# Kernel optimization log

Hardware: AMD Instinct MI355X
Metric: run time of the kernel (lower is better)

Reference implementation:

```python
import jax, jax.numpy as jnp
import numpy as np
from jax import lax

D, R, C = 4, 6, 32
P = 2 * R + 1
N = P * P
MR = 12
MP = 2 * MR + 1
MN = MP * MP


def corr_sampler(f_t, f_r, r, dilate):
    # SpatialCorrelationSampler(kernel_size=1, patch_size=2r+1, dilation_patch=dilate)
    # out[b,py,px,y,x] = sum_c f_t[b,c,y,x] * f_r[b,c, y+(py-r)*dilate, x+(px-r)*dilate] (zero pad)
    b, c, h, w = f_t.shape
    p = 2 * r + 1
    pad = r * dilate
    f_r_p = jnp.pad(f_r, ((0, 0), (0, 0), (pad, pad), (pad, pad)))
    offs = jnp.arange(p, dtype=jnp.int32) * dilate
    ii, jj = jnp.meshgrid(offs, offs, indexing='ij')
    shifts = jnp.stack([ii.ravel(), jj.ravel()], 1)  # (p*p, 2)

    def step(_, ij):
        win = lax.dynamic_slice(f_r_p, (0, 0, ij[0], ij[1]), (b, c, h, w))
        return None, jnp.sum(f_t * win, axis=1)  # (b,h,w)

    _, out = lax.scan(step, None, shifts)  # (p*p, b, h, w)
    return out.transpose(1, 0, 2, 3).reshape(b, p, p, h, w)


def bilinear_sample(im, xs, ys):
    # im: (b,c,H,W); xs, ys: (b,h,w) pixel coords; zero padding outside (grid_sample semantics)
    b, c, H, W = im.shape
    x0 = jnp.floor(xs)
    y0 = jnp.floor(ys)
    out = jnp.zeros((b, c) + xs.shape[1:], im.dtype)
    for dy in (0.0, 1.0):
        for dx in (0.0, 1.0):
            xi = x0 + dx
            yi = y0 + dy
            wgt = (1.0 - jnp.abs(xs - xi)) * (1.0 - jnp.abs(ys - yi))
            valid = (xi >= 0) & (xi <= W - 1) & (yi >= 0) & (yi <= H - 1)
            xc = jnp.clip(xi, 0, W - 1).astype(jnp.int32)
            yc = jnp.clip(yi, 0, H - 1).astype(jnp.int32)
            v = jax.vmap(lambda imb, yb, xb: imb[:, yb, xb])(im, yc, xc)  # (b,c,h,w)
            out = out + v * (wgt * valid.astype(im.dtype))[:, None]
    return out


def deform_im2col(im, offset, r):
    # im: (b,c,h,w); offset: (b,h,w,2) with channels (x, y)
    # returns (b, c, (2r+1)^2, h, w), kernel positions row-major over (ky, kx)
    b, c, H, W = im.shape
    h, w = offset.shape[1], offset.shape[2]
    bx = jnp.arange(W, dtype=im.dtype)[None, None, :] + offset[..., 0]  # (b,h,w)
    by = jnp.arange(H, dtype=im.dtype)[None, :, None] + offset[..., 1]
    ks = jnp.arange(-r, r + 1, dtype=im.dtype)
    ky, kx = jnp.meshgrid(ks, ks, indexing='ij')
    koff = jnp.stack([ky.ravel(), kx.ravel()], 1)  # (N, 2) as (ky, kx)

    def step(_, k):
        return None, bilinear_sample(im, bx + k[1], by + k[0])  # (b,c,h,w)

    _, cols = lax.scan(step, None, koff)  # (N,b,c,h,w)
    return cols.transpose(1, 2, 0, 3, 4)


def unfold(x, r):
    # F.unfold(x, kernel_size=2r+1, padding=r) reshaped to (b,c,N,h,w)
    b, c, h, w = x.shape
    p = 2 * r + 1
    xp = jnp.pad(x, ((0, 0), (0, 0), (r, r), (r, r)))
    iy = jnp.arange(p)[:, None] + jnp.arange(h)[None, :]  # (p,h)
    ix = jnp.arange(p)[:, None] + jnp.arange(w)[None, :]  # (p,w)
    win = xp[:, :, iy[:, None, :, None], ix[None, :, None, :]]  # (b,c,p,p,h,w)
    return win.reshape(b, c, p * p, h, w)


def colorizer_forward(feats_r, feats_t, quantized_r, ref_index, current_ind, dil_int):
    ref_list = [int(v) for v in np.asarray(ref_index)]
    nref = feats_r.shape[0]
    gaps = [int(current_ind) - x for x in ref_list]
    nsearch = len([g for g in gaps if g > int(dil_int)])
    dirates = [min(4, g // int(dil_int) + 1) for g in gaps if g > int(dil_int)]
    b, c, h, w = feats_t.shape

    gy, gx = jnp.meshgrid(jnp.arange(-MR, MR + 1, dtype=feats_t.dtype),
                          jnp.arange(-MR, MR + 1, dtype=feats_t.dtype), indexing='ij')
    grid = jnp.stack([gx, gy], -1).reshape(1, MP, MP, 1, 1, 2)

    corrs = []
    offset0 = None
    for i in range(nsearch):
        cc = corr_sampler(feats_t, feats_r[i], MR, dirates[i])  # (b,MP,MP,h,w)
        cc = jax.nn.softmax(cc.reshape(b, MN, h * w), axis=1)
        cc = cc.reshape(b, MP, MP, h, w, 1)
        # expected displacement (x, y); NOTE: original code keeps only the LAST offset0
        offset0 = (cc * grid).sum(axis=(1, 2)) * dirates[i]  # (b,h,w,2)
        col0 = deform_im2col(feats_r[i], offset0, R)  # (b,c,N,h,w)
        corr = (feats_t[:, :, None] * col0).sum(axis=1).reshape(b, N, h * w)
        corrs.append(corr)
    for i in range(nsearch, nref):
        cr = corr_sampler(feats_t, feats_r[i], R, 1).reshape(b, N, h * w)
        corrs.append(cr)

    corr = jax.nn.softmax(jnp.concatenate(corrs, 1), axis=1)[:, None]  # (b,1,nref*N,hw)

    qr = [quantized_r[i][:, :, ::D, ::D] for i in range(nref)]  # prep: stride D (C!=1)
    cols = [deform_im2col(qr[i], offset0, R).reshape(b, C, N, h * w) for i in range(nsearch)]
    cols += [unfold(qr[i], R).reshape(b, C, N, h * w) for i in range(nsearch, nref)]
    image_uf = jnp.concatenate(cols, 2)  # (b,C,nref*N,hw)

    out = (corr * image_uf).sum(axis=2).reshape(b, C, h, w)
    return out


def setup_inputs() -> dict:
    key = jax.random.key(0)
    k1, k2, k3 = jax.random.split(key, 3)
    feats_r = jax.random.normal(k1, (3, 2, 64, 48, 48), jnp.float32) * 0.1
    feats_t = jax.random.normal(k2, (2, 64, 48, 48), jnp.float32) * 0.1
    quantized_r = jax.random.normal(k3, (3, 2, 32, 192, 192), jnp.float32)
    ref_index = np.array([0, 20, 35], dtype=np.int64)
    return {"feats_r": feats_r, "feats_t": feats_t, "quantized_r": quantized_r,
            "ref_index": ref_index, "current_ind": 40, "dil_int": 15}


def reference(feats_r, feats_t, quantized_r, ref_index, current_ind, dil_int):
    return colorizer_forward(feats_r, feats_t, quantized_r, ref_index, current_ind, dil_int)
```

## Files before the change

kernel.cpp:

```cpp
#include <hip/hip_runtime.h>


typedef unsigned short ushort_t;
typedef unsigned int uint_t;
typedef __attribute__((ext_vector_type(8))) short short8;
typedef __attribute__((ext_vector_type(4))) float f32x4;

namespace {
constexpr int NPIX = 2304;
constexpr int FC   = 64;
constexpr int QC   = 32;

constexpr size_t OFS_FTB  = 0;
constexpr size_t OFS_FRB  = OFS_FTB + (size_t)2*NPIX*FC*2;
constexpr size_t OFS_QRCL = OFS_FRB + (size_t)6*NPIX*FC*2;
constexpr size_t OFS_ACC  = OFS_QRCL + (size_t)6*NPIX*QC*4;
constexpr size_t OFS_CORB = OFS_ACC + (size_t)4*NPIX*16*4;
}

__device__ __forceinline__ ushort_t f2b(float f) {
  uint_t u = __float_as_uint(f);
  return (ushort_t)((u + 0x7fffu + ((u >> 16) & 1u)) >> 16);
}

__global__ __launch_bounds__(256) void pack_all(const float* __restrict__ ft,
                                                const float* __restrict__ fr,
                                                const float* __restrict__ q,
                                                ushort_t* __restrict__ ftb,
                                                ushort_t* __restrict__ frb,
                                                float* __restrict__ qrcl) {
  const int bid = blockIdx.x;
  const int tid = threadIdx.x;
  if (bid < 288) {
    __shared__ float lds[64][65];
    const int mat = bid / 36;
    const int p0  = (bid % 36) * 64;
    const float* src = (mat < 2) ? (ft + (size_t)mat * FC * NPIX)
                                 : (fr + (size_t)(mat - 2) * FC * NPIX);
    ushort_t* dst = (mat < 2) ? (ftb + (size_t)mat * NPIX * FC)
                              : (frb + (size_t)(mat - 2) * NPIX * FC);
    const int lane = tid & 63, row = tid >> 6;
    #pragma unroll
    for (int ch = row; ch < 64; ch += 4)
      lds[ch][lane] = src[(size_t)ch * NPIX + p0 + lane];
    __syncthreads();
    #pragma unroll
    for (int p = row; p < 64; p += 4)
      dst[(size_t)(p0 + p) * FC + lane] = f2b(lds[lane][p]);
  } else {
    __shared__ float lq[32][49];
    const int zz = bid - 288;
    const int ib = zz / 48, yy = zz % 48;
    const float* src = q + (size_t)ib * 32 * 36864 + (size_t)(4 * yy) * 192;
    #pragma unroll
    for (int k = 0; k < 6; ++k) {
      const int l = tid + k * 256;
      const int ch = l / 48, xx = l % 48;
      lq[ch][xx] = src[(size_t)ch * 36864 + 4 * xx];
    }
    __syncthreads();
    float* dst = qrcl + ((size_t)ib * NPIX + yy * 48) * QC;
    #pragma unroll
    for (int k = 0; k < 6; ++k) {
      const int o = tid + k * 256;
      dst[o] = lq[o & 31][o >> 5];
    }
  }
}

template<int MODE>
__device__ __forceinline__ void gram_body(const ushort_t* __restrict__ ftb,
                                          const ushort_t* __restrict__ frb,
                                          float* __restrict__ accb,
                                          float* __restrict__ corb,
                                          int y, int m0, int b, int chunk,
                                          int c0, int c1) {
  constexpr int D_  = (MODE == 0) ? 3 : (MODE == 1) ? 2 : 1;
  constexpr int RAD = (MODE == 2) ? 6 : 12;

  const int lane = threadIdx.x;
  const int col  = lane & 15;
  const int kg   = lane >> 4;

  const short8* ftv = (const short8*)(ftb + ((size_t)b * NPIX + y * 48 + m0 + col) * FC);
  short8 aF0 = ftv[kg];
  short8 aF1 = ftv[4 + kg];

  float wm[3][4], dxv[3][4];
  int sbase[3][4];
  #pragma unroll
  for (int nt = 0; nt < 3; ++nt) {
    #pragma unroll
    for (int r = 0; r < 4; ++r) {
      const int xr   = m0 + kg * 4 + r;
      const int diff = nt * 16 + col - xr;
      const int qd   = diff / D_;
      const bool v   = (diff % D_ == 0) && (qd >= -RAD) && (qd <= RAD);
      wm[nt][r]  = v ? 1.f : 0.f;
      dxv[nt][r] = (float)qd;
      if (MODE == 2) sbase[nt][r] = ((int)b * NPIX + y * 48 + xr) * 169 + (qd + 6);
    }
  }

  const ushort_t* frmat = frb + (size_t)(MODE * 2 + b) * NPIX * FC;
  float se[4] = {0,0,0,0}, sx[4] = {0,0,0,0}, sy[4] = {0,0,0,0};

  for (int dy = c0; dy < c1; ++dy) {
    const int yyr = y + (dy - RAD) * D_;
    if (yyr < 0 || yyr >= 48) continue;
    const float dyv = (float)(dy - RAD);
    const short8* frow = (const short8*)(frmat + (size_t)yyr * 48 * FC);
    #pragma unroll
    for (int nt = 0; nt < 3; ++nt) {
      const short8* bp = frow + (size_t)(nt * 16 + col) * 8;
      short8 b0 = bp[kg], b1 = bp[4 + kg];
      f32x4 c = {0.f, 0.f, 0.f, 0.f};
      c = __builtin_amdgcn_mfma_f32_16x16x32_bf16(aF0, b0, c, 0, 0, 0);
      c = __builtin_amdgcn_mfma_f32_16x16x32_bf16(aF1, b1, c, 0, 0, 0);
      if (MODE < 2) {
        #pragma unroll
        for (int r = 0; r < 4; ++r) {
          const float e = __expf(c[r]) * wm[nt][r];
          se[r] += e;
          sx[r] = fmaf(e, dxv[nt][r], sx[r]);
          sy[r] = fmaf(e, dyv, sy[r]);
        }
      } else {
        #pragma unroll
        for (int r = 0; r < 4; ++r)
          if (wm[nt][r] != 0.f) corb[sbase[nt][r] + dy * 13] = c[r];
      }
    }
  }

  if (MODE < 2) {
    #pragma unroll
    for (int r = 0; r < 4; ++r) {
      #pragma unroll
      for (int m = 1; m <= 8; m <<= 1) {
        se[r] += __shfl_xor(se[r], m);
        sx[r] += __shfl_xor(sx[r], m);
        sy[r] += __shfl_xor(sy[r], m);
      }
    }
    if (col == 0) {
      #pragma unroll
      for (int r = 0; r < 4; ++r) {
        const int p = y * 48 + m0 + kg * 4 + r;
        float* a = accb + ((size_t)(MODE * 2 + b) * NPIX + p) * 16 + chunk * 3;
        a[0] = se[r]; a[1] = sx[r]; a[2] = sy[r];
      }
    }
  }
}

__global__ __launch_bounds__(64) void gram_kernel(const ushort_t* __restrict__ ftb,
                                                  const ushort_t* __restrict__ frb,
                                                  float* __restrict__ accb,
                                                  float* __restrict__ corb) {
  const int y  = ((blockIdx.x & 7) * 6) + (blockIdx.x >> 3);
  const int m0 = blockIdx.y * 16;
  const int z  = blockIdx.z;
  if (z < 10) {
    const int b = z / 5, chunk = z % 5;
    gram_body<0>(ftb, frb, accb, corb, y, m0, b, chunk, chunk * 5, chunk * 5 + 5);
  } else if (z < 20) {
    const int zz = z - 10;
    const int b = zz / 5, chunk = zz % 5;
    gram_body<1>(ftb, frb, accb, corb, y, m0, b, chunk, chunk * 5, chunk * 5 + 5);
  } else {
    const int zz = z - 20;
    const int b = zz / 3, chunk = zz % 3;
    const int c0 = (chunk == 0) ? 0 : (chunk == 1) ? 5 : 9;
    const int c1 = (chunk == 0) ? 5 : (chunk == 1) ? 9 : 13;
    gram_body<2>(ftb, frb, accb, corb, y, m0, b, chunk, c0, c1);
  }
}

__global__ __launch_bounds__(128, 6) void fuse_kernel(const ushort_t* __restrict__ ftb,
                                                      const ushort_t* __restrict__ frb,
                                                      const float* __restrict__ accb,
                                                      const float* __restrict__ corb,
                                                      const float* __restrict__ qrcl,
                                                      float* __restrict__ out) {
  const int tid = threadIdx.x;
  const int wv = tid >> 6, lane = tid & 63;
  const int b = blockIdx.y;
  const int bsw = ((blockIdx.x & 7) * 144) + (blockIdx.x >> 3);
  const int pix = bsw * 2 + wv;
  const int x = pix % 48, y = pix / 48;

  __shared__ __align__(16) float sDu[2][416];
  __shared__ float sp[2][512];
  __shared__ int   gaddr[2][224];
  __shared__ float gw0[2][224], gw1[2][224];

  const int kgB = lane >> 4;
  const short8* ftv = (const short8*)(ftb + ((size_t)b * NPIX + pix) * FC);
  const short8 bF0 = ftv[kgB], bF1 = ftv[4 + kgB];

  float cv5 = 0.f, cv6 = 0.f, cv7 = 0.f;
  {
    const float* cb = corb + ((size_t)b * NPIX + pix) * 169;
    int n = lane - 18;
    if (n >= 0) {
      const int yy = y + n / 13 - 6, xx = x + n % 13 - 6;
      if (yy >= 0 && yy < 48 && xx >= 0 && xx < 48) cv5 = cb[n];
    }
    n = lane + 46;
    {
      const int yy = y + n / 13 - 6, xx = x + n % 13 - 6;
      if (yy >= 0 && yy < 48 && xx >= 0 && xx < 48) cv6 = cb[n];
    }
    n = lane + 110;
    if (n < 169) {
      const int yy = y + n / 13 - 6, xx = x + n % 13 - 6;
      if (yy >= 0 && yy < 48 && xx >= 0 && xx < 48) cv7 = cb[n];
    }
  }

  float vox = 0.f, voy = 0.f;
  if (lane < 2) {
    const int d = (lane == 0) ? 3 : 2;
    const float4* a4 = (const float4*)(accb + ((size_t)(lane * 2 + b) * NPIX + pix) * 16);
    float t[16];
    *(float4*)&t[0]  = a4[0]; *(float4*)&t[4]  = a4[1];
    *(float4*)&t[8]  = a4[2]; *(float4*)&t[12] = a4[3];
    float se = t[0] + t[3] + t[6] + t[9] + t[12];
    float sx = t[1] + t[4] + t[7] + t[10] + t[13];
    float sy = t[2] + t[5] + t[8] + t[11] + t[14];
    const int klox = max(-12, -(x / d)), khix = min(12, (47 - x) / d);
    const int kloy = max(-12, -(y / d)), khiy = min(12, (47 - y) / d);
    const int nvx = khix - klox + 1, nvy = khiy - kloy + 1;
    const int svx = (klox + khix) * nvx / 2, svy = (kloy + khiy) * nvy / 2;
    se += (float)(625 - nvx * nvy);
    sx -= (float)(nvy * svx);
    sy -= (float)(nvx * svy);
    vox = (float)d * sx / se;
    voy = (float)d * sy / se;
  }
  const float ox0 = __shfl(vox, 0), oy0 = __shfl(voy, 0);
  const float ox1 = __shfl(vox, 1), oy1 = __shfl(voy, 1);

  const float bxf0 = floorf((float)x + ox0), byf0 = floorf((float)y + oy0);
  const float bxf1 = floorf((float)x + ox1), byf1 = floorf((float)y + oy1);
  const float fx0 = (float)x + ox0 - bxf0, fy0 = (float)y + oy0 - byf0;
  const float fx1 = (float)x + ox1 - bxf1, fy1 = (float)y + oy1 - byf1;
  const int bx00 = (int)bxf0 - 6, by00 = (int)byf0 - 6;
  const int bx01 = (int)bxf1 - 6, by01 = (int)byf1 - 6;

  {
    const int arow = lane & 15, kg = lane >> 4;
    const short8 z8 = {0,0,0,0,0,0,0,0};
    float* sDw = sDu[wv];
    #pragma unroll 2
    for (int gi = 0; gi < 26; ++gi) {
      const bool r1 = gi >= 13;
      const int grp = r1 ? gi - 13 : gi;
      const int g = grp * 16 + arow;
      short8 a0 = z8, a1 = z8;
      if (g < 196) {
        const int gy = (r1 ? by01 : by00) + g / 14;
        const int gx = (r1 ? bx01 : bx00) + g % 14;
        if (gy >= 0 && gy < 48 && gx >= 0 && gx < 48) {
          const short8* fp = (const short8*)(frb + ((size_t)((r1 ? 2 : 0) + b) * NPIX + gy * 48 + gx) * FC);
          a0 = fp[kg]; a1 = fp[4 + kg];
        }
      }
      f32x4 c = {0.f, 0.f, 0.f, 0.f};
      c = __builtin_amdgcn_mfma_f32_16x16x32_bf16(a0, bF0, c, 0, 0, 0);
      c = __builtin_amdgcn_mfma_f32_16x16x32_bf16(a1, bF1, c, 0, 0, 0);
      if (arow == 0)
        *(f32x4*)&sDw[(r1 ? 208 : 0) + grp * 16 + kg * 4] = c;
    }
  }
  __syncthreads();

  float ls = 0.f;
  {
    float* spw = sp[wv];
    const float* sD0 = sDu[wv];
    const float* sD1 = sDu[wv] + 208;
    #pragma unroll
    for (int k = 0; k < 8; ++k) {
      const int s = lane + 64 * k;
      if (s < 507) {
        float v;
        if (s < 338) {
          const bool r1 = (s >= 169);
          const unsigned n = r1 ? s - 169 : s;
          const float fx = r1 ? fx1 : fx0, fy = r1 ? fy1 : fy0;
          const float w00 = (1.f - fy) * (1.f - fx), w01 = (1.f - fy) * fx;
          const float w10 = fy * (1.f - fx),        w11 = fy * fx;
          const unsigned a_ = n / 13u, c2 = n % 13u;
          const float* Dp = r1 ? sD1 : sD0;
          v = w00 * Dp[a_ * 14 + c2]       + w01 * Dp[a_ * 14 + c2 + 1]
            + w10 * Dp[(a_ + 1) * 14 + c2] + w11 * Dp[(a_ + 1) * 14 + c2 + 1];
        } else {
          v = (k == 5) ? cv5 : (k == 6) ? cv6 : cv7;
        }
        const float e = __expf(v);
        spw[s] = e; ls += e;
      }
    }
  }
  #pragma unroll
  for (int o = 1; o <= 32; o <<= 1) ls += __shfl_xor(ls, o);
  const float inv = 1.f / ls;
  __syncthreads();

  int*   gaddr2 = (int*)sDu[wv];
  float* gwq2   = sDu[wv] + 208;
  {
    const float* spw = sp[wv];
    const float w00 = (1.f - fy1) * (1.f - fx1), w01 = (1.f - fy1) * fx1;
    const float w10 = fy1 * (1.f - fx1),        w11 = fy1 * fx1;
    #pragma unroll
    for (int j = 0; j < 4; ++j) {
      const int t = lane + 64 * j;
      if (t < 224) {
        if (t < 196) {
          const int ty = t / 14, tx = t % 14;
          auto P = [&](const float* base, int a, int c2) -> float {
            return (a >= 0 && a < 13 && c2 >= 0 && c2 < 13) ? base[a * 13 + c2] : 0.f;
          };
          const float s0 = w00 * P(spw, ty, tx)     + w01 * P(spw, ty, tx - 1)
                         + w10 * P(spw, ty - 1, tx) + w11 * P(spw, ty - 1, tx - 1);
          const float s1 = w00 * P(spw + 169, ty, tx)     + w01 * P(spw + 169, ty, tx - 1)
                         + w10 * P(spw + 169, ty - 1, tx) + w11 * P(spw + 169, ty - 1, tx - 1);
          const int gy = by01 + ty, gx = bx01 + tx;
          const bool v = (gy >= 0 && gy < 48 && gx >= 0 && gx < 48);
          gaddr[wv][t] = v ? (gy * 48 + gx) * QC : 0;
          gw0[wv][t] = v ? s0 : 0.f;
          gw1[wv][t] = v ? s1 : 0.f;
        } else {
          gaddr[wv][t] = 0; gw0[wv][t] = 0.f; gw1[wv][t] = 0.f;
        }
      }
    }
    #pragma unroll
    for (int j = 0; j < 3; ++j) {
      const int t = lane + 64 * j;
      if (t < 169) {
        const int yy = y + t / 13 - 6, xx = x + t % 13 - 6;
        const bool v = (yy >= 0 && yy < 48 && xx >= 0 && xx < 48);
        gaddr2[t] = v ? (yy * 48 + xx) * QC : 0;
        gwq2[t] = v ? spw[338 + t] : 0.f;
      } else {
        gaddr2[t] = 0; gwq2[t] = 0.f;
      }
    }
  }
  __syncthreads();

  const int chgrp = lane & 7, ssub = lane >> 3;
  const float* q0 = qrcl + (size_t)(0 + b) * NPIX * QC + chgrp * 4;
  const float* q1 = qrcl + (size_t)(2 + b) * NPIX * QC + chgrp * 4;
  const float* q2 = qrcl + (size_t)(4 + b) * NPIX * QC + chgrp * 4;
  float4 acc = {0.f, 0.f, 0.f, 0.f};
  const int* ga = gaddr[wv];
  const float* w0p = gw0[wv];
  const float* w1p = gw1[wv];
  #pragma unroll 4
  for (int it = 0; it < 28; ++it) {
    const int s = it * 8 + ssub;
    const int a = ga[s];
    const float w0 = w0p[s], w1 = w1p[s];
    const float4 v0 = *(const float4*)(q0 + a);
    const float4 v1 = *(const float4*)(q1 + a);
    acc.x = fmaf(w0, v0.x, acc.x); acc.y = fmaf(w0, v0.y, acc.y);
    acc.z = fmaf(w0, v0.z, acc.z); acc.w = fmaf(w0, v0.w, acc.w);
    acc.x = fmaf(w1, v1.x, acc.x); acc.y = fmaf(w1, v1.y, acc.y);
    acc.z = fmaf(w1, v1.z, acc.z); acc.w = fmaf(w1, v1.w, acc.w);
  }
  #pragma unroll 4
  for (int it = 0; it < 24; ++it) {
    const int s = it * 8 + ssub;
    const int a = gaddr2[s];
    const float w = gwq2[s];
    const float4 v2 = *(const float4*)(q2 + a);
    acc.x = fmaf(w, v2.x, acc.x); acc.y = fmaf(w, v2.y, acc.y);
    acc.z = fmaf(w, v2.z, acc.z); acc.w = fmaf(w, v2.w, acc.w);
  }
  #pragma unroll
  for (int off = 8; off <= 32; off <<= 1) {
    acc.x += __shfl_xor(acc.x, off);
    acc.y += __shfl_xor(acc.y, off);
    acc.z += __shfl_xor(acc.z, off);
    acc.w += __shfl_xor(acc.w, off);
  }
  if (ssub == 0) {
    float* op = out + ((size_t)(b * 32 + chgrp * 4) * 48 + y) * 48 + x;
    op[0]        = acc.x * inv;
    op[NPIX]     = acc.y * inv;
    op[2 * NPIX] = acc.z * inv;
    op[3 * NPIX] = acc.w * inv;
  }
}

extern "C" void kernel_launch(void* const* d_in, const int* in_sizes, int n_in,
                              void* d_out, int out_size, void* d_ws, size_t ws_size,
                              hipStream_t stream) {
  (void)in_sizes; (void)n_in; (void)out_size; (void)ws_size;
  const float* feats_r     = (const float*)d_in[0];
  const float* feats_t     = (const float*)d_in[1];
  const float* quantized_r = (const float*)d_in[2];
  char* ws = (char*)d_ws;
  ushort_t* ftb  = (ushort_t*)(ws + OFS_FTB);
  ushort_t* frb  = (ushort_t*)(ws + OFS_FRB);
  float*    qrcl = (float*)(ws + OFS_QRCL);
  float*    accb = (float*)(ws + OFS_ACC);
  float*    corb = (float*)(ws + OFS_CORB);

  pack_all<<<576, 256, 0, stream>>>(feats_t, feats_r, quantized_r, ftb, frb, qrcl);
  gram_kernel<<<dim3(48, 3, 26), 64, 0, stream>>>(ftb, frb, accb, corb);
  fuse_kernel<<<dim3(NPIX / 2, 2), 128, 0, stream>>>(ftb, frb, accb, corb, qrcl, (float*)d_out);
}
```

Measured before the change: 138.6 us.

## Move quantized repack into gram kernel and use one-wave fuse blocks

The strided quantized-feature repack moves out of the first pack kernel into extra z-slices of the gram kernel, so it runs alongside the MFMA correlation work instead of ahead of it. The fuse kernel changes from two-wave blocks (two pixels each) to single-wave blocks with one pixel, using half the shared memory per block and a different pixel swizzle. The aim is to shorten the critical path of the first launch and let blocks finish more independently. In exchange, each repack block now has 64 threads doing 24 iterations, and the fuse kernel launches twice as many blocks.

```diff
diff --git a/kernel.cpp b/kernel.cpp
--- a/kernel.cpp
+++ b/kernel.cpp
@@ -23,49 +23,26 @@
   return (ushort_t)((u + 0x7fffu + ((u >> 16) & 1u)) >> 16);
 }
 
-__global__ __launch_bounds__(256) void pack_all(const float* __restrict__ ft,
-                                                const float* __restrict__ fr,
-                                                const float* __restrict__ q,
-                                                ushort_t* __restrict__ ftb,
-                                                ushort_t* __restrict__ frb,
-                                                float* __restrict__ qrcl) {
-  const int bid = blockIdx.x;
+__global__ __launch_bounds__(256) void pack_feats(const float* __restrict__ ft,
+                                                  const float* __restrict__ fr,
+                                                  ushort_t* __restrict__ ftb,
+                                                  ushort_t* __restrict__ frb) {
+  __shared__ float lds[64][65];
   const int tid = threadIdx.x;
-  if (bid < 288) {
-    __shared__ float lds[64][65];
-    const int mat = bid / 36;
-    const int p0  = (bid % 36) * 64;
-    const float* src = (mat < 2) ? (ft + (size_t)mat * FC * NPIX)
-                                 : (fr + (size_t)(mat - 2) * FC * NPIX);
-    ushort_t* dst = (mat < 2) ? (ftb + (size_t)mat * NPIX * FC)
-                              : (frb + (size_t)(mat - 2) * NPIX * FC);
-    const int lane = tid & 63, row = tid >> 6;
-    #pragma unroll
-    for (int ch = row; ch < 64; ch += 4)
-      lds[ch][lane] = src[(size_t)ch * NPIX + p0 + lane];
-    __syncthreads();
-    #pragma unroll
-    for (int p = row; p < 64; p += 4)
-      dst[(size_t)(p0 + p) * FC + lane] = f2b(lds[lane][p]);
-  } else {
-    __shared__ float lq[32][49];
-    const int zz = bid - 288;
-    const int ib = zz / 48, yy = zz % 48;
-    const float* src = q + (size_t)ib * 32 * 36864 + (size_t)(4 * yy) * 192;
-    #pragma unroll
-    for (int k = 0; k < 6; ++k) {
-      const int l = tid + k * 256;
-      const int ch = l / 48, xx = l % 48;
-      lq[ch][xx] = src[(size_t)ch * 36864 + 4 * xx];
-    }
-    __syncthreads();
-    float* dst = qrcl + ((size_t)ib * NPIX + yy * 48) * QC;
-    #pragma unroll
-    for (int k = 0; k < 6; ++k) {
-      const int o = tid + k * 256;
-      dst[o] = lq[o & 31][o >> 5];
-    }
-  }
+  const int mat = blockIdx.x / 36;
+  const int p0  = (blockIdx.x % 36) * 64;
+  const float* src = (mat < 2) ? (ft + (size_t)mat * FC * NPIX)
+                               : (fr + (size_t)(mat - 2) * FC * NPIX);
+  ushort_t* dst = (mat < 2) ? (ftb + (size_t)mat * NPIX * FC)
+                            : (frb + (size_t)(mat - 2) * NPIX * FC);
+  const int lane = tid & 63, row = tid >> 6;
+  #pragma unroll
+  for (int ch = row; ch < 64; ch += 4)
+    lds[ch][lane] = src[(size_t)ch * NPIX + p0 + lane];
+  __syncthreads();
+  #pragma unroll
+  for (int p = row; p < 64; p += 4)
+    dst[(size_t)(p0 + p) * FC + lane] = f2b(lds[lane][p]);
 }
 
 template<int MODE>
@@ -156,11 +133,34 @@
 
 __global__ __launch_bounds__(64) void gram_kernel(const ushort_t* __restrict__ ftb,
                                                   const ushort_t* __restrict__ frb,
+                                                  const float* __restrict__ q,
                                                   float* __restrict__ accb,
-                                                  float* __restrict__ corb) {
+                                                  float* __restrict__ corb,
+                                                  float* __restrict__ qrcl) {
+  const int z = blockIdx.z;
+  if (z >= 26) {
+    __shared__ float lq[32][49];
+    const int tid = threadIdx.x;
+    const int ib = (z - 26) * 3 + blockIdx.y;
+    const int yy = blockIdx.x;
+    const float* src = q + (size_t)ib * 32 * 36864 + (size_t)(4 * yy) * 192;
+    #pragma unroll
+    for (int k = 0; k < 24; ++k) {
+      const int l = tid + k * 64;
+      const int ch = l / 48, xx = l % 48;
+      lq[ch][xx] = src[(size_t)ch * 36864 + 4 * xx];
+    }
+    __syncthreads();
+    float* dst = qrcl + ((size_t)ib * NPIX + yy * 48) * QC;
+    #pragma unroll
+    for (int k = 0; k < 24; ++k) {
+      const int o = tid + k * 64;
+      dst[o] = lq[o & 31][o >> 5];
+    }
+    return;
+  }
   const int y  = ((blockIdx.x & 7) * 6) + (blockIdx.x >> 3);
   const int m0 = blockIdx.y * 16;
-  const int z  = blockIdx.z;
   if (z < 10) {
     const int b = z / 5, chunk = z % 5;
     gram_body<0>(ftb, frb, accb, corb, y, m0, b, chunk, chunk * 5, chunk * 5 + 5);
@@ -177,23 +177,21 @@
   }
 }
 
-__global__ __launch_bounds__(128, 6) void fuse_kernel(const ushort_t* __restrict__ ftb,
-                                                      const ushort_t* __restrict__ frb,
-                                                      const float* __restrict__ accb,
-                                                      const float* __restrict__ corb,
-                                                      const float* __restrict__ qrcl,
-                                                      float* __restrict__ out) {
-  const int tid = threadIdx.x;
-  const int wv = tid >> 6, lane = tid & 63;
+__global__ __launch_bounds__(64, 4) void fuse_kernel(const ushort_t* __restrict__ ftb,
+                                                     const ushort_t* __restrict__ frb,
+                                                     const float* __restrict__ accb,
+                                                     const float* __restrict__ corb,
+                                                     const float* __restrict__ qrcl,
+                                                     float* __restrict__ out) {
+  const int lane = threadIdx.x;
   const int b = blockIdx.y;
-  const int bsw = ((blockIdx.x & 7) * 144) + (blockIdx.x >> 3);
-  const int pix = bsw * 2 + wv;
+  const int pix = ((blockIdx.x & 7) * 288) + (blockIdx.x >> 3);
   const int x = pix % 48, y = pix / 48;
 
-  __shared__ __align__(16) float sDu[2][416];
-  __shared__ float sp[2][512];
-  __shared__ int   gaddr[2][224];
-  __shared__ float gw0[2][224], gw1[2][224];
+  __shared__ __align__(16) float sDu[416];
+  __shared__ float sp[512];
+  __shared__ int   gaddr[224];
+  __shared__ float gw0[224], gw1[224];
 
   const int kgB = lane >> 4;
   const short8* ftv = (const short8*)(ftb + ((size_t)b * NPIX + pix) * FC);
@@ -252,7 +250,6 @@
   {
     const int arow = lane & 15, kg = lane >> 4;
     const short8 z8 = {0,0,0,0,0,0,0,0};
-    float* sDw = sDu[wv];
     #pragma unroll 2
     for (int gi = 0; gi < 26; ++gi) {
       const bool r1 = gi >= 13;
@@ -271,16 +268,15 @@
       c = __builtin_amdgcn_mfma_f32_16x16x32_bf16(a0, bF0, c, 0, 0, 0);
       c = __builtin_amdgcn_mfma_f32_16x16x32_bf16(a1, bF1, c, 0, 0, 0);
       if (arow == 0)
-        *(f32x4*)&sDw[(r1 ? 208 : 0) + grp * 16 + kg * 4] = c;
+        *(f32x4*)&sDu[(r1 ? 208 : 0) + grp * 16 + kg * 4] = c;
     }
   }
   __syncthreads();
 
   float ls = 0.f;
   {
-    float* spw = sp[wv];
-    const float* sD0 = sDu[wv];
-    const float* sD1 = sDu[wv] + 208;
+    const float* sD0 = sDu;
+    const float* sD1 = sDu + 208;
     #pragma unroll
     for (int k = 0; k < 8; ++k) {
       const int s = lane + 64 * k;
@@ -300,7 +296,7 @@
           v = (k == 5) ? cv5 : (k == 6) ? cv6 : cv7;
         }
         const float e = __expf(v);
-        spw[s] = e; ls += e;
+        sp[s] = e; ls += e;
       }
     }
   }
@@ -309,10 +305,9 @@
   const float inv = 1.f / ls;
   __syncthreads();
 
-  int*   gaddr2 = (int*)sDu[wv];
-  float* gwq2   = sDu[wv] + 208;
+  int*   gaddr2 = (int*)sDu;
+  float* gwq2   = sDu + 208;
   {
-    const float* spw = sp[wv];
     const float w00 = (1.f - fy1) * (1.f - fx1), w01 = (1.f - fy1) * fx1;
     const float w10 = fy1 * (1.f - fx1),        w11 = fy1 * fx1;
     #pragma unroll
@@ -324,17 +319,17 @@
           auto P = [&](const float* base, int a, int c2) -> float {
             return (a >= 0 && a < 13 && c2 >= 0 && c2 < 13) ? base[a * 13 + c2] : 0.f;
           };
-          const float s0 = w00 * P(spw, ty, tx)     + w01 * P(spw, ty, tx - 1)
-                         + w10 * P(spw, ty - 1, tx) + w11 * P(spw, ty - 1, tx - 1);
-          const float s1 = w00 * P(spw + 169, ty, tx)     + w01 * P(spw + 169, ty, tx - 1)
-                         + w10 * P(spw + 169, ty - 1, tx) + w11 * P(spw + 169, ty - 1, tx - 1);
+          const float s0 = w00 * P(sp, ty, tx)     + w01 * P(sp, ty, tx - 1)
+                         + w10 * P(sp, ty - 1, tx) + w11 * P(sp, ty - 1, tx - 1);
+          const float s1 = w00 * P(sp + 169, ty, tx)     + w01 * P(sp + 169, ty, tx - 1)
+                         + w10 * P(sp + 169, ty - 1, tx) + w11 * P(sp + 169, ty - 1, tx - 1);
           const int gy = by01 + ty, gx = bx01 + tx;
           const bool v = (gy >= 0 && gy < 48 && gx >= 0 && gx < 48);
-          gaddr[wv][t] = v ? (gy * 48 + gx) * QC : 0;
-          gw0[wv][t] = v ? s0 : 0.f;
-          gw1[wv][t] = v ? s1 : 0.f;
+          gaddr[t] = v ? (gy * 48 + gx) * QC : 0;
+          gw0[t] = v ? s0 : 0.f;
+          gw1[t] = v ? s1 : 0.f;
         } else {
-          gaddr[wv][t] = 0; gw0[wv][t] = 0.f; gw1[wv][t] = 0.f;
+          gaddr[t] = 0; gw0[t] = 0.f; gw1[t] = 0.f;
         }
       }
     }
@@ -345,7 +340,7 @@
         const int yy = y + t / 13 - 6, xx = x + t % 13 - 6;
         const bool v = (yy >= 0 && yy < 48 && xx >= 0 && xx < 48);
         gaddr2[t] = v ? (yy * 48 + xx) * QC : 0;
-        gwq2[t] = v ? spw[338 + t] : 0.f;
+        gwq2[t] = v ? sp[338 + t] : 0.f;
       } else {
         gaddr2[t] = 0; gwq2[t] = 0.f;
       }
@@ -358,14 +353,11 @@
   const float* q1 = qrcl + (size_t)(2 + b) * NPIX * QC + chgrp * 4;
   const float* q2 = qrcl + (size_t)(4 + b) * NPIX * QC + chgrp * 4;
   float4 acc = {0.f, 0.f, 0.f, 0.f};
-  const int* ga = gaddr[wv];
-  const float* w0p = gw0[wv];
-  const float* w1p = gw1[wv];
   #pragma unroll 4
   for (int it = 0; it < 28; ++it) {
     const int s = it * 8 + ssub;
-    const int a = ga[s];
-    const float w0 = w0p[s], w1 = w1p[s];
+    const int a = gaddr[s];
+    const float w0 = gw0[s], w1 = gw1[s];
     const float4 v0 = *(const float4*)(q0 + a);
     const float4 v1 = *(const float4*)(q1 + a);
     acc.x = fmaf(w0, v0.x, acc.x); acc.y = fmaf(w0, v0.y, acc.y);
@@ -412,7 +404,7 @@
   float*    accb = (float*)(ws + OFS_ACC);
   float*    corb = (float*)(ws + OFS_CORB);
 
-  pack_all<<<576, 256, 0, stream>>>(feats_t, feats_r, quantized_r, ftb, frb, qrcl);
-  gram_kernel<<<dim3(48, 3, 26), 64, 0, stream>>>(ftb, frb, accb, corb);
-  fuse_kernel<<<dim3(NPIX / 2, 2), 128, 0, stream>>>(ftb, frb, accb, corb, qrcl, (float*)d_out);
-}
+  pack_feats<<<288, 256, 0, stream>>>(feats_t, feats_r, ftb, frb);
+  gram_kernel<<<dim3(48, 3, 28), 64, 0, stream>>>(ftb, frb, quantized_r, accb, corb, qrcl);
+  fuse_kernel<<<dim3(NPIX, 2), 64, 0, stream>>>(ftb, frb, accb, corb, qrcl, (float*)d_out);
+}
```

Result: no change. 139.7 us (+0.8%).
